# Optimization experiments

Measured on AMD Instinct MI355X. Metric: run time of the kernel, lower is better.

## Reference

```python
import jax, jax.numpy as jnp
import numpy as np

EMB_DIM = 1024
HEAD_DIM = 64


def setup_inputs() -> dict:
    key = jax.random.key(0)
    kx, kq, kk, kv = jax.random.split(key, 4)
    B, S = 4, 4096
    x = jax.random.normal(kx, (B, S, EMB_DIM), dtype=jnp.float32)
    # nn.Linear weights are [out, in]; kaiming-uniform-ish init scale
    lim = 1.0 / np.sqrt(EMB_DIM)
    Wq = jax.random.uniform(kq, (HEAD_DIM, EMB_DIM), jnp.float32, -lim, lim)
    Wk = jax.random.uniform(kk, (HEAD_DIM, EMB_DIM), jnp.float32, -lim, lim)
    Wv = jax.random.uniform(kv, (HEAD_DIM, EMB_DIM), jnp.float32, -lim, lim)
    return {"x": x, "Wq": Wq, "Wk": Wk, "Wv": Wv}


def reference(x, Wq, Wk, Wv):
    # x: [B, S, E]; W*: [H, E] (torch Linear layout) -> project with x @ W.T
    Q = jnp.einsum("bse,he->bsh", x, Wq)
    K = jnp.einsum("bse,he->bsh", x, Wk)
    V = jnp.einsum("bse,he->bsh", x, Wv)
    # NOTE: source scales by emb_dim**0.5, not head_dim**0.5 — keep faithful.
    scores = jnp.einsum("bqh,bkh->bqk", Q, K) / jnp.sqrt(jnp.float32(x.shape[-1]))
    S = scores.shape[-1]
    causal = jnp.tril(jnp.ones((S, S), dtype=bool))  # [S, S]
    scores = jnp.where(causal, scores, -jnp.inf)
    attn = jax.nn.softmax(scores, axis=-1)
    return jnp.einsum("bqk,bkh->bqh", attn, V)
```

## Files before the change

### kernel.cpp

```cpp
#include <hip/hip_runtime.h>
#include <hip/hip_bf16.h>
#include <math.h>

#define B_ 4
#define S_ 4096
#define E_ 1024

typedef __attribute__((ext_vector_type(8))) short bf16x8;
typedef __attribute__((ext_vector_type(4))) short bf16x4;
typedef __attribute__((ext_vector_type(4))) float f32x4;

__device__ __forceinline__ unsigned short f2bf(float f) {
  unsigned u = __float_as_uint(f);
  u = u + 0x7fffu + ((u >> 16) & 1u);
  return (unsigned short)(u >> 16);
}

__global__ __launch_bounds__(256) void proj_kernel(
    const float* __restrict__ x, const float* __restrict__ Wq,
    const float* __restrict__ Wk, const float* __restrict__ Wv,
    unsigned short* __restrict__ Qp, unsigned short* __restrict__ Kb,
    unsigned short* __restrict__ Vt)
{
  __shared__ __align__(16) unsigned short xs[64*64];
  __shared__ __align__(16) unsigned short wl[192*64];
  const int tid = threadIdx.x;
  const int wave = tid >> 6, lane = tid & 63;
  const int l15 = lane & 15, l4 = lane >> 4;
  const int m0 = blockIdx.x * 64;

  f32x4 acc[12];
  #pragma unroll
  for (int i = 0; i < 12; i++) acc[i] = (f32x4)0.f;

  f32x4 xr[4], wr[12];
  #pragma unroll
  for (int i = 0; i < 4; i++) {
    int c = tid + i*256; int row = c >> 4, cc = c & 15;
    xr[i] = *(const f32x4*)(x + (size_t)(m0 + row)*E_ + cc*4);
  }
  #pragma unroll
  for (int i = 0; i < 12; i++) {
    int c = tid + i*256; int n = c >> 4, cc = c & 15;
    const float* Wsrc = (n < 64) ? (Wq + (size_t)n*E_)
                     : ((n < 128) ? (Wk + (size_t)(n-64)*E_)
                                  : (Wv + (size_t)(n-128)*E_));
    wr[i] = *(const f32x4*)(Wsrc + cc*4);
  }

  for (int ks = 0; ks < 16; ks++) {
    __syncthreads();
    #pragma unroll
    for (int i = 0; i < 4; i++) {
      int c = tid + i*256; int row = c >> 4, cc = c & 15;
      bf16x4 v;
      v[0] = (short)f2bf(xr[i][0]); v[1] = (short)f2bf(xr[i][1]);
      v[2] = (short)f2bf(xr[i][2]); v[3] = (short)f2bf(xr[i][3]);
      *(bf16x4*)((char*)xs + row*128 + ((cc*8) ^ ((row&7)<<4))) = v;
    }
    #pragma unroll
    for (int i = 0; i < 12; i++) {
      int c = tid + i*256; int n = c >> 4, cc = c & 15;
      bf16x4 v;
      v[0] = (short)f2bf(wr[i][0]); v[1] = (short)f2bf(wr[i][1]);
      v[2] = (short)f2bf(wr[i][2]); v[3] = (short)f2bf(wr[i][3]);
      *(bf16x4*)((char*)wl + n*128 + ((cc*8) ^ ((n&7)<<4))) = v;
    }
    if (ks < 15) {
      #pragma unroll
      for (int i = 0; i < 4; i++) {
        int c = tid + i*256; int row = c >> 4, cc = c & 15;
        xr[i] = *(const f32x4*)(x + (size_t)(m0 + row)*E_ + (ks+1)*64 + cc*4);
      }
      #pragma unroll
      for (int i = 0; i < 12; i++) {
        int c = tid + i*256; int n = c >> 4, cc = c & 15;
        const float* Wsrc = (n < 64) ? (Wq + (size_t)n*E_)
                         : ((n < 128) ? (Wk + (size_t)(n-64)*E_)
                                      : (Wv + (size_t)(n-128)*E_));
        wr[i] = *(const f32x4*)(Wsrc + (ks+1)*64 + cc*4);
      }
    }
    __syncthreads();
    const int arow = wave*16 + l15;
    const int aswz = (arow&7)<<4;
    bf16x8 a0 = *(const bf16x8*)((const char*)xs + arow*128 + ((l4*16) ^ aswz));
    bf16x8 a1 = *(const bf16x8*)((const char*)xs + arow*128 + ((64 + l4*16) ^ aswz));
    #pragma unroll
    for (int ntl = 0; ntl < 12; ntl++) {
      int brow = ntl*16 + l15;
      int bswz = (brow&7)<<4;
      bf16x8 b0 = *(const bf16x8*)((const char*)wl + brow*128 + ((l4*16) ^ bswz));
      bf16x8 b1 = *(const bf16x8*)((const char*)wl + brow*128 + ((64 + l4*16) ^ bswz));
      acc[ntl] = __builtin_amdgcn_mfma_f32_16x16x32_bf16(a0, b0, acc[ntl], 0, 0, 0);
      acc[ntl] = __builtin_amdgcn_mfma_f32_16x16x32_bf16(a1, b1, acc[ntl], 0, 0, 0);
    }
  }

  const float QSC = 0.04508422f;
  const int mb = m0 + wave*16 + l4*4;
  #pragma unroll
  for (int ntl = 0; ntl < 4; ntl++) {
    int col = ntl*16 + l15;
    #pragma unroll
    for (int r = 0; r < 4; r++)
      Qp[(size_t)(mb + r)*64 + col] = f2bf(acc[ntl][r] * QSC);
  }
  #pragma unroll
  for (int ntl = 0; ntl < 4; ntl++) {
    int col = ntl*16 + l15;
    #pragma unroll
    for (int r = 0; r < 4; r++)
      Kb[(size_t)(mb + r)*64 + col] = f2bf(acc[4+ntl][r]);
  }
  const int b = m0 >> 12;
  const int sb = (m0 & 4095) + wave*16 + l4*4;
  #pragma unroll
  for (int ntl = 0; ntl < 4; ntl++) {
    int d = ntl*16 + l15;
    bf16x4 v;
    #pragma unroll
    for (int r = 0; r < 4; r++) v[r] = (short)f2bf(acc[8+ntl][r]);
    *(bf16x4*)(Vt + (size_t)(b*64 + d)*S_ + sb) = v;
  }
}

__global__ __launch_bounds__(256) void attn_kernel(
    const unsigned short* __restrict__ Qp,
    const unsigned short* __restrict__ Kb,
    const unsigned short* __restrict__ Vt,
    float* __restrict__ out)
{
  __shared__ __align__(16) unsigned short Ks[64*64];
  __shared__ __align__(16) unsigned short Vs[64*64];
  __shared__ __align__(16) float mergeO[4][16][64];
  __shared__ float mstats[4][16][2];

  const int tid = threadIdx.x;
  const int wave = tid >> 6, lane = tid & 63;
  const int l15 = lane & 15, l4 = lane >> 4;
  const int g = wave >> 1, h = wave & 1;

  const int bid = blockIdx.x;
  const int u = bid >> 1, par = bid & 1;
  const int b = u & 3;
  const int pp = u >> 2;
  const int jq = par ? (127 - pp) : pp;

  const unsigned short* Qb  = Qp + (size_t)b*S_*64;
  const unsigned short* Kbb = Kb + (size_t)b*S_*64;
  const unsigned short* Vtb = Vt + (size_t)b*64*S_;
  float* outb = out + (size_t)b*S_*64;

  const int q0 = jq * 32;
  const int ntile = (jq >> 1) + 1;
  const int qrow = q0 + g*16 + l15;

  bf16x8 qf0 = *(const bf16x8*)(Qb + (size_t)qrow*64 + l4*8);
  bf16x8 qf1 = *(const bf16x8*)(Qb + (size_t)qrow*64 + 32 + l4*8);

  float m = -INFINITY, lsum = 0.f;
  f32x4 acc[4];
  #pragma unroll
  for (int i = 0; i < 4; i++) acc[i] = (f32x4)0.f;

  f32x4 kreg[2], vreg[2];
  #pragma unroll
  for (int i = 0; i < 2; i++) {
    int c = tid + i*256; int row = c >> 3, cc = c & 7;
    kreg[i] = *(const f32x4*)((const char*)Kbb + (size_t)row*128 + cc*16);
    vreg[i] = *(const f32x4*)((const char*)Vtb + (size_t)row*8192 + cc*16);
  }

  for (int t = 0; t < ntile; t++) {
    __syncthreads();
    #pragma unroll
    for (int i = 0; i < 2; i++) {
      int c = tid + i*256; int row = c >> 3, cc = c & 7;
      *(f32x4*)((char*)Ks + row*128 + ((cc*16) ^ ((row&7)<<4))) = kreg[i];
      *(f32x4*)((char*)Vs + row*128 + ((cc*16) ^ ((row&7)<<4))) = vreg[i];
    }
    if (t + 1 < ntile) {
      int k0 = (t+1)*64;
      #pragma unroll
      for (int i = 0; i < 2; i++) {
        int c = tid + i*256; int row = c >> 3, cc = c & 7;
        kreg[i] = *(const f32x4*)((const char*)Kbb + (size_t)(k0+row)*128 + cc*16);
        vreg[i] = *(const f32x4*)((const char*)Vtb + (size_t)row*8192 + (size_t)k0*2 + cc*16);
      }
    }
    __syncthreads();

    f32x4 sv[2];
    #pragma unroll
    for (int st = 0; st < 2; st++) {
      int krow = (2*h + st)*16 + l15;
      const char* kbp = (const char*)Ks + krow*128;
      int swz = (krow&7)<<4;
      bf16x8 k0f = *(const bf16x8*)(kbp + ((l4*16) ^ swz));
      bf16x8 k1f = *(const bf16x8*)(kbp + ((64 + l4*16) ^ swz));
      f32x4 z = (f32x4)0.f;
      z = __builtin_amdgcn_mfma_f32_16x16x32_bf16(k0f, qf0, z, 0, 0, 0);
      z = __builtin_amdgcn_mfma_f32_16x16x32_bf16(k1f, qf1, z, 0, 0, 0);
      sv[st] = z;
    }
    if (t == ntile - 1) {
      #pragma unroll
      for (int st = 0; st < 2; st++) {
        #pragma unroll
        for (int r = 0; r < 4; r++) {
          int kg = t*64 + (2*h + st)*16 + l4*4 + r;
          if (kg > qrow) sv[st][r] = -INFINITY;
        }
      }
    }
    float pmax = sv[0][0];
    #pragma unroll
    for (int st = 0; st < 2; st++) {
      #pragma unroll
      for (int r = 0; r < 4; r++) pmax = fmaxf(pmax, sv[st][r]);
    }
    pmax = fmaxf(pmax, __shfl_xor(pmax, 16, 64));
    pmax = fmaxf(pmax, __shfl_xor(pmax, 32, 64));
    float mnew = fmaxf(m, pmax);
    float msafe = (mnew == -INFINITY) ? 0.f : mnew;
    float scale = exp2f(m - msafe);
    float pv[8]; float psum = 0.f;
    #pragma unroll
    for (int i = 0; i < 8; i++) {
      pv[i] = exp2f(sv[i>>2][i&3] - msafe);
      psum += pv[i];
    }
    psum += __shfl_xor(psum, 16, 64);
    psum += __shfl_xor(psum, 32, 64);
    lsum = lsum*scale + psum;
    m = mnew;
    #pragma unroll
    for (int i = 0; i < 4; i++) acc[i] *= scale;
    bf16x8 pf;
    #pragma unroll
    for (int i = 0; i < 8; i++) pf[i] = (short)f2bf(pv[i]);
    #pragma unroll
    for (int dt = 0; dt < 4; dt++) {
      int drow = dt*16 + l15;
      const char* vb = (const char*)Vs + drow*128;
      int swz = (drow&7)<<4;
      bf16x4 v0 = *(const bf16x4*)(vb + ((h*64 + l4*8) ^ swz));
      bf16x4 v1 = *(const bf16x4*)(vb + ((h*64 + 32 + l4*8) ^ swz));
      bf16x8 vf;
      #pragma unroll
      for (int i = 0; i < 4; i++) { vf[i] = v0[i]; vf[i+4] = v1[i]; }
      acc[dt] = __builtin_amdgcn_mfma_f32_16x16x32_bf16(vf, pf, acc[dt], 0, 0, 0);
    }
  }

  __syncthreads();
  #pragma unroll
  for (int dt = 0; dt < 4; dt++)
    *(f32x4*)&mergeO[wave][l15][dt*16 + l4*4] = acc[dt];
  if (lane < 16) { mstats[wave][lane][0] = m; mstats[wave][lane][1] = lsum; }
  __syncthreads();
  {
    int ql = tid >> 3, dc = tid & 7;
    int gg = ql >> 4, q16 = ql & 15;
    float m1 = mstats[gg*2+0][q16][0], s1 = mstats[gg*2+0][q16][1];
    float m2 = mstats[gg*2+1][q16][0], s2 = mstats[gg*2+1][q16][1];
    float m12 = fmaxf(m1, m2);
    float a1 = exp2f(m1 - m12), a2 = exp2f(m2 - m12);
    float inv = 1.f / (s1*a1 + s2*a2);
    a1 *= inv; a2 *= inv;
    #pragma unroll
    for (int i = 0; i < 2; i++) {
      int d = dc*8 + i*4;
      f32x4 o1 = *(const f32x4*)&mergeO[gg*2+0][q16][d];
      f32x4 o2 = *(const f32x4*)&mergeO[gg*2+1][q16][d];
      f32x4 o = o1*a1 + o2*a2;
      *(f32x4*)(outb + (size_t)(q0 + ql)*64 + d) = o;
    }
  }
}

extern "C" void kernel_launch(void* const* d_in, const int* in_sizes, int n_in,
                              void* d_out, int out_size, void* d_ws, size_t ws_size,
                              hipStream_t stream)
{
  const float* x  = (const float*)d_in[0];
  const float* Wq = (const float*)d_in[1];
  const float* Wk = (const float*)d_in[2];
  const float* Wv = (const float*)d_in[3];
  unsigned short* Qp  = (unsigned short*)d_ws;
  unsigned short* Kbp = Qp  + (size_t)B_*S_*64;
  unsigned short* Vtp = Kbp + (size_t)B_*S_*64;
  float* out = (float*)d_out;

  hipLaunchKernelGGL(proj_kernel, dim3(256), dim3(256), 0, stream,
                     x, Wq, Wk, Wv, Qp, Kbp, Vtp);
  hipLaunchKernelGGL(attn_kernel, dim3(512), dim3(256), 0, stream,
                     Qp, Kbp, Vtp, out);
}
```

Baseline: 173.3 us.

## Load K/V fragments directly from global into registers, drop LDS staging

```diff
diff --git a/kernel.cpp b/kernel.cpp
--- a/kernel.cpp
+++ b/kernel.cpp
@@ -131,9 +131,7 @@
     const unsigned short* __restrict__ Vt,
     float* __restrict__ out)
 {
-  __shared__ __align__(16) unsigned short Ks[64*64];
-  __shared__ __align__(16) unsigned short Vs[64*64];
-  __shared__ __align__(16) float mergeO[4][16][64];
+  __shared__ __align__(16) float mergeO[4][16][68];
   __shared__ float mstats[4][16][2];
 
   const int tid = threadIdx.x;
@@ -164,95 +162,89 @@
   #pragma unroll
   for (int i = 0; i < 4; i++) acc[i] = (f32x4)0.f;
 
-  f32x4 kreg[2], vreg[2];
-  #pragma unroll
-  for (int i = 0; i < 2; i++) {
-    int c = tid + i*256; int row = c >> 3, cc = c & 7;
-    kreg[i] = *(const f32x4*)((const char*)Kbb + (size_t)row*128 + cc*16);
-    vreg[i] = *(const f32x4*)((const char*)Vtb + (size_t)row*8192 + cc*16);
-  }
-
-  for (int t = 0; t < ntile; t++) {
-    __syncthreads();
-    #pragma unroll
-    for (int i = 0; i < 2; i++) {
-      int c = tid + i*256; int row = c >> 3, cc = c & 7;
-      *(f32x4*)((char*)Ks + row*128 + ((cc*16) ^ ((row&7)<<4))) = kreg[i];
-      *(f32x4*)((char*)Vs + row*128 + ((cc*16) ^ ((row&7)<<4))) = vreg[i];
-    }
+  bf16x8 kfA[4], kfB[4];
+  bf16x4 vfA[8], vfB[8];
+
+  #define LOADF(KF, VF, tt) do {                                               \
+    _Pragma("unroll")                                                          \
+    for (int st = 0; st < 2; st++) {                                           \
+      const unsigned short* kp =                                               \
+          Kbb + (size_t)((tt)*64 + (2*h + st)*16 + l15)*64 + l4*8;             \
+      KF[st*2+0] = *(const bf16x8*)kp;                                         \
+      KF[st*2+1] = *(const bf16x8*)(kp + 32);                                  \
+    }                                                                          \
+    _Pragma("unroll")                                                          \
+    for (int dt = 0; dt < 4; dt++) {                                           \
+      const unsigned short* vp =                                               \
+          Vtb + (size_t)(dt*16 + l15)*S_ + (tt)*64 + h*32 + l4*4;              \
+      VF[dt*2+0] = *(const bf16x4*)vp;                                         \
+      VF[dt*2+1] = *(const bf16x4*)(vp + 16);                                  \
+    }                                                                          \
+  } while (0)
+
+  #define COMPUTE(KF, VF, tt) do {                                             \
+    f32x4 sv0 = (f32x4)0.f, sv1 = (f32x4)0.f;                                  \
+    sv0 = __builtin_amdgcn_mfma_f32_16x16x32_bf16(KF[0], qf0, sv0, 0, 0, 0);   \
+    sv0 = __builtin_amdgcn_mfma_f32_16x16x32_bf16(KF[1], qf1, sv0, 0, 0, 0);   \
+    sv1 = __builtin_amdgcn_mfma_f32_16x16x32_bf16(KF[2], qf0, sv1, 0, 0, 0);   \
+    sv1 = __builtin_amdgcn_mfma_f32_16x16x32_bf16(KF[3], qf1, sv1, 0, 0, 0);   \
+    if ((tt) == ntile - 1) {                                                   \
+      _Pragma("unroll")                                                        \
+      for (int r = 0; r < 4; r++) {                                            \
+        int kg0 = (tt)*64 + (2*h + 0)*16 + l4*4 + r;                           \
+        int kg1 = (tt)*64 + (2*h + 1)*16 + l4*4 + r;                           \
+        if (kg0 > qrow) sv0[r] = -INFINITY;                                    \
+        if (kg1 > qrow) sv1[r] = -INFINITY;                                    \
+      }                                                                        \
+    }                                                                          \
+    float pmax = sv0[0];                                                       \
+    _Pragma("unroll")                                                          \
+    for (int r = 0; r < 4; r++) {                                              \
+      pmax = fmaxf(pmax, sv0[r]); pmax = fmaxf(pmax, sv1[r]);                  \
+    }                                                                          \
+    pmax = fmaxf(pmax, __shfl_xor(pmax, 16, 64));                              \
+    pmax = fmaxf(pmax, __shfl_xor(pmax, 32, 64));                              \
+    float mnew = fmaxf(m, pmax);                                               \
+    float msafe = (mnew == -INFINITY) ? 0.f : mnew;                            \
+    float scale = exp2f(m - msafe);                                            \
+    float pv[8]; float psum = 0.f;                                             \
+    _Pragma("unroll")                                                          \
+    for (int i = 0; i < 8; i++) {                                              \
+      float s = (i < 4) ? sv0[i & 3] : sv1[i & 3];                             \
+      pv[i] = exp2f(s - msafe);                                                \
+      psum += pv[i];                                                           \
+    }                                                                          \
+    psum += __shfl_xor(psum, 16, 64);                                          \
+    psum += __shfl_xor(psum, 32, 64);                                          \
+    lsum = lsum*scale + psum;                                                  \
+    m = mnew;                                                                  \
+    _Pragma("unroll")                                                          \
+    for (int i = 0; i < 4; i++) acc[i] *= scale;                               \
+    bf16x8 pf;                                                                 \
+    _Pragma("unroll")                                                          \
+    for (int i = 0; i < 8; i++) pf[i] = (short)f2bf(pv[i]);                    \
+    _Pragma("unroll")                                                          \
+    for (int dt = 0; dt < 4; dt++) {                                           \
+      bf16x8 vf;                                                               \
+      _Pragma("unroll")                                                        \
+      for (int i = 0; i < 4; i++) {                                            \
+        vf[i] = VF[dt*2+0][i]; vf[i+4] = VF[dt*2+1][i];                        \
+      }                                                                        \
+      acc[dt] = __builtin_amdgcn_mfma_f32_16x16x32_bf16(vf, pf, acc[dt], 0, 0, 0); \
+    }                                                                          \
+  } while (0)
+
+  LOADF(kfA, vfA, 0);
+  for (int t = 0; t < ntile; t += 2) {
+    if (t + 1 < ntile) LOADF(kfB, vfB, t + 1);
+    COMPUTE(kfA, vfA, t);
     if (t + 1 < ntile) {
-      int k0 = (t+1)*64;
-      #pragma unroll
-      for (int i = 0; i < 2; i++) {
-        int c = tid + i*256; int row = c >> 3, cc = c & 7;
-        kreg[i] = *(const f32x4*)((const char*)Kbb + (size_t)(k0+row)*128 + cc*16);
-        vreg[i] = *(const f32x4*)((const char*)Vtb + (size_t)row*8192 + (size_t)k0*2 + cc*16);
-      }
-    }
-    __syncthreads();
-
-    f32x4 sv[2];
-    #pragma unroll
-    for (int st = 0; st < 2; st++) {
-      int krow = (2*h + st)*16 + l15;
-      const char* kbp = (const char*)Ks + krow*128;
-      int swz = (krow&7)<<4;
-      bf16x8 k0f = *(const bf16x8*)(kbp + ((l4*16) ^ swz));
-      bf16x8 k1f = *(const bf16x8*)(kbp + ((64 + l4*16) ^ swz));
-      f32x4 z = (f32x4)0.f;
-      z = __builtin_amdgcn_mfma_f32_16x16x32_bf16(k0f, qf0, z, 0, 0, 0);
-      z = __builtin_amdgcn_mfma_f32_16x16x32_bf16(k1f, qf1, z, 0, 0, 0);
-      sv[st] = z;
-    }
-    if (t == ntile - 1) {
-      #pragma unroll
-      for (int st = 0; st < 2; st++) {
-        #pragma unroll
-        for (int r = 0; r < 4; r++) {
-          int kg = t*64 + (2*h + st)*16 + l4*4 + r;
-          if (kg > qrow) sv[st][r] = -INFINITY;
-        }
-      }
-    }
-    float pmax = sv[0][0];
-    #pragma unroll
-    for (int st = 0; st < 2; st++) {
-      #pragma unroll
-      for (int r = 0; r < 4; r++) pmax = fmaxf(pmax, sv[st][r]);
-    }
-    pmax = fmaxf(pmax, __shfl_xor(pmax, 16, 64));
-    pmax = fmaxf(pmax, __shfl_xor(pmax, 32, 64));
-    float mnew = fmaxf(m, pmax);
-    float msafe = (mnew == -INFINITY) ? 0.f : mnew;
-    float scale = exp2f(m - msafe);
-    float pv[8]; float psum = 0.f;
-    #pragma unroll
-    for (int i = 0; i < 8; i++) {
-      pv[i] = exp2f(sv[i>>2][i&3] - msafe);
-      psum += pv[i];
-    }
-    psum += __shfl_xor(psum, 16, 64);
-    psum += __shfl_xor(psum, 32, 64);
-    lsum = lsum*scale + psum;
-    m = mnew;
-    #pragma unroll
-    for (int i = 0; i < 4; i++) acc[i] *= scale;
-    bf16x8 pf;
-    #pragma unroll
-    for (int i = 0; i < 8; i++) pf[i] = (short)f2bf(pv[i]);
-    #pragma unroll
-    for (int dt = 0; dt < 4; dt++) {
-      int drow = dt*16 + l15;
-      const char* vb = (const char*)Vs + drow*128;
-      int swz = (drow&7)<<4;
-      bf16x4 v0 = *(const bf16x4*)(vb + ((h*64 + l4*8) ^ swz));
-      bf16x4 v1 = *(const bf16x4*)(vb + ((h*64 + 32 + l4*8) ^ swz));
-      bf16x8 vf;
-      #pragma unroll
-      for (int i = 0; i < 4; i++) { vf[i] = v0[i]; vf[i+4] = v1[i]; }
-      acc[dt] = __builtin_amdgcn_mfma_f32_16x16x32_bf16(vf, pf, acc[dt], 0, 0, 0);
-    }
-  }
+      if (t + 2 < ntile) LOADF(kfA, vfA, t + 2);
+      COMPUTE(kfB, vfB, t + 1);
+    }
+  }
+  #undef LOADF
+  #undef COMPUTE
 
   __syncthreads();
   #pragma unroll
```

New measurement: 266.8 us. 1.54x slower.
